# Kernel optimization log

Measured on AMD Instinct MI355X. Metric: run time of the kernel, lower is better.

The kernel has to match this reference:

```python
import jax, jax.numpy as jnp
import numpy as np

K = 5
TAU = 0.5
N = 8192
IN_DIM = 128
OUT_DIM = 128


def setup_inputs() -> dict:
    key = jax.random.key(0)
    k1, k2, k3 = jax.random.split(key, 3)
    x = jax.random.normal(k1, (N, IN_DIM), dtype=jnp.float32)
    laplacian = jax.random.normal(k2, (N, N), dtype=jnp.float32) / np.sqrt(N)
    # xavier-uniform-like init for theta (K, in_dim, out_dim)
    limit = np.sqrt(6.0 / (IN_DIM + OUT_DIM))
    theta = jax.random.uniform(k3, (K, IN_DIM, OUT_DIM), dtype=jnp.float32,
                               minval=-limit, maxval=limit)
    return {"x": x, "laplacian": laplacian, "theta": theta}


def _cheb_coeff(k_order: int, tau: float) -> jnp.ndarray:
    # c_k = (2/K) * exp(-tau * cos(pi*(k+0.5)/K)), Chebyshev-Gauss nodes
    ks = jnp.arange(k_order, dtype=jnp.float32)
    x_k = jnp.cos(jnp.pi * (ks + 0.5) / k_order)
    return (2.0 / k_order) * jnp.exp(-tau * x_k)


def reference(x, laplacian, theta):
    coeff = _cheb_coeff(K, TAU)  # (K,)
    # Chebyshev recurrence: T_0 = x, T_1 = L x, T_k = 2 L T_{k-1} - T_{k-2}
    tx_prev, tx_curr = x, laplacian @ x
    tx_list = [tx_prev, tx_curr]
    for _ in range(2, K):
        tx_next = 2.0 * (laplacian @ tx_curr) - tx_prev
        tx_list.append(tx_next)
        tx_prev, tx_curr = tx_curr, tx_next
    tx_stack = jnp.stack(tx_list, axis=0)  # (K, N, in_dim)
    return jnp.einsum('kni,kio,k->no', tx_stack, theta, coeff)
```

## Files before the change

### kernel.cpp

```cpp
#include <hip/hip_runtime.h>
#include <hip/hip_bf16.h>
#include <cmath>

#define NROWS 8192
#define DIM   128
#define KDIM  8192
#define BM    64
#define BN    128
#define BK    64
#define SPLITK 8
#define KCHUNK (KDIM / SPLITK)
#define GITERS (KCHUNK / BK)
#define LDSTRIDE 80

typedef __bf16 bf16_t;
typedef __bf16 bf16x8 __attribute__((ext_vector_type(8)));
typedef __bf16 bf16x4 __attribute__((ext_vector_type(4)));
typedef float  f32x4  __attribute__((ext_vector_type(4)));

__device__ __forceinline__ void async16(const void* g, void* l) {
    __builtin_amdgcn_global_load_lds(
        (const __attribute__((address_space(1))) unsigned int*)g,
        (__attribute__((address_space(3))) unsigned int*)l, 16, 0, 0);
}

__global__ void k_cvtL(const float* __restrict__ src, bf16_t* __restrict__ dst) {
    size_t i = ((size_t)blockIdx.x * 256 + threadIdx.x) * 8;
    float4 a = *(const float4*)(src + i);
    float4 b = *(const float4*)(src + i + 4);
    bf16x8 v;
    v[0] = (bf16_t)a.x; v[1] = (bf16_t)a.y; v[2] = (bf16_t)a.z; v[3] = (bf16_t)a.w;
    v[4] = (bf16_t)b.x; v[5] = (bf16_t)b.y; v[6] = (bf16_t)b.z; v[7] = (bf16_t)b.w;
    *(bf16x8*)(dst + i) = v;
}

__global__ void k_theta(const float* __restrict__ th, bf16_t* __restrict__ out,
                        float c0, float c1, float c2, float c3, float c4) {
    int idx = blockIdx.x * 256 + threadIdx.x;
    int k = idx >> 14;
    int o = (idx >> 7) & 127;
    int i = idx & 127;
    float c = (k == 0) ? c0 : (k == 1) ? c1 : (k == 2) ? c2 : (k == 3) ? c3 : c4;
    out[idx] = (bf16_t)(c * th[(k << 14) + (i << 7) + o]);
}

__global__ __launch_bounds__(256, 3)
void k_gemm(const bf16_t* __restrict__ A, const bf16_t* __restrict__ Bt,
            float* __restrict__ partial) {
    __shared__ __align__(16) bf16_t As[2][BM * BK];
    __shared__ __align__(16) bf16_t Bs[2][BN * BK];

    const int t     = threadIdx.x;
    const int mTile = blockIdx.x & 127;
    const int s     = blockIdx.x >> 7;
    const int mb    = mTile * BM;
    const int k0base = s * KCHUNK;
    const int wave = t >> 6, lane = t & 63;
    const int wM = (wave & 1) * 32;
    const int wN = (wave >> 1) * 64;
    const int lm = lane & 15, lk = lane >> 4;
    const int lrow = lane >> 3;
    const int lsrc = (lane & 7) ^ lrow;

    f32x4 acc[2][4];
#pragma unroll
    for (int a = 0; a < 2; ++a)
#pragma unroll
        for (int b = 0; b < 4; ++b) acc[a][b] = (f32x4)0.0f;

    auto stage = [&](int kk, int buf) {
        const int k0 = k0base + kk * BK;
#pragma unroll
        for (int i = 0; i < 2; ++i) {
            const int r = wave * 16 + i * 8 + lrow;
            async16(A + (size_t)(mb + r) * KDIM + k0 + lsrc * 8,
                    &As[buf][(wave * 16 + i * 8) * BK]);
        }
#pragma unroll
        for (int i = 0; i < 4; ++i) {
            const int n = wave * 32 + i * 8 + lrow;
            async16(Bt + (size_t)n * KDIM + k0 + lsrc * 8,
                    &Bs[buf][(wave * 32 + i * 8) * BK]);
        }
    };

    stage(0, 0);
    __syncthreads();
    for (int kk = 0; kk < GITERS; ++kk) {
        const int buf = kk & 1;
        if (kk + 1 < GITERS) stage(kk + 1, buf ^ 1);
#pragma unroll
        for (int ko = 0; ko < 2; ++ko) {
            bf16x8 af[2], bfr[4];
            const int csX = (ko * 4 + lk) ^ (lm & 7);
#pragma unroll
            for (int tm = 0; tm < 2; ++tm) {
                const int r = wM + tm * 16 + lm;
                af[tm] = *(const bf16x8*)(&As[buf][r * BK + csX * 8]);
            }
#pragma unroll
            for (int tn = 0; tn < 4; ++tn) {
                const int n = wN + tn * 16 + lm;
                bfr[tn] = *(const bf16x8*)(&Bs[buf][n * BK + csX * 8]);
            }
#pragma unroll
            for (int tm = 0; tm < 2; ++tm)
#pragma unroll
                for (int tn = 0; tn < 4; ++tn)
                    acc[tm][tn] = __builtin_amdgcn_mfma_f32_16x16x32_bf16(
                        af[tm], bfr[tn], acc[tm][tn], 0, 0, 0);
        }
        __syncthreads();
    }

    float* pOut = partial + (size_t)s * NROWS * DIM;
#pragma unroll
    for (int tm = 0; tm < 2; ++tm)
#pragma unroll
        for (int tn = 0; tn < 4; ++tn)
#pragma unroll
            for (int r = 0; r < 4; ++r) {
                const int row = mb + wM + tm * 16 + lk * 4 + r;
                const int col = wN + tn * 16 + lm;
                pOut[(size_t)row * DIM + col] = acc[tm][tn][r];
            }
}

template <int MODE>
__global__ void k_combine(const float* __restrict__ src, const float* __restrict__ prev,
                          float* __restrict__ f32dst, bf16_t* __restrict__ tbf,
                          bf16_t* __restrict__ bt) {
    __shared__ bf16_t tl[128 * 24];
    const size_t S = (size_t)NROWS * DIM;
    const int t  = threadIdx.x;
    const int n0 = blockIdx.x * 16;
    const int nl = t >> 4;
    const int dp = (t & 15) * 8;
    const int n  = n0 + nl;

    float y[8];
    if (MODE == 0) {
        float4 a = *(const float4*)(src + (size_t)n * DIM + dp);
        float4 b = *(const float4*)(src + (size_t)n * DIM + dp + 4);
        y[0] = a.x; y[1] = a.y; y[2] = a.z; y[3] = a.w;
        y[4] = b.x; y[5] = b.y; y[6] = b.z; y[7] = b.w;
    } else {
#pragma unroll
        for (int j = 0; j < 8; ++j) y[j] = 0.0f;
#pragma unroll
        for (int ss = 0; ss < SPLITK; ++ss) {
            const float* p = src + (size_t)ss * S + (size_t)n * DIM + dp;
            float4 a = *(const float4*)p;
            float4 b = *(const float4*)(p + 4);
            y[0] += a.x; y[1] += a.y; y[2] += a.z; y[3] += a.w;
            y[4] += b.x; y[5] += b.y; y[6] += b.z; y[7] += b.w;
        }
        if (MODE == 2) {
            float4 a = *(const float4*)(prev + (size_t)n * DIM + dp);
            float4 b = *(const float4*)(prev + (size_t)n * DIM + dp + 4);
            y[0] = 2.0f * y[0] - a.x; y[1] = 2.0f * y[1] - a.y;
            y[2] = 2.0f * y[2] - a.z; y[3] = 2.0f * y[3] - a.w;
            y[4] = 2.0f * y[4] - b.x; y[5] = 2.0f * y[5] - b.y;
            y[6] = 2.0f * y[6] - b.z; y[7] = 2.0f * y[7] - b.w;
        }
    }
    if (f32dst) {
        float4 a, b;
        a.x = y[0]; a.y = y[1]; a.z = y[2]; a.w = y[3];
        b.x = y[4]; b.y = y[5]; b.z = y[6]; b.w = y[7];
        *(float4*)(f32dst + (size_t)n * DIM + dp) = a;
        *(float4*)(f32dst + (size_t)n * DIM + dp + 4) = b;
    }
    bf16x8 v;
#pragma unroll
    for (int j = 0; j < 8; ++j) v[j] = (bf16_t)y[j];
    *(bf16x8*)(tbf + (size_t)n * DIM + dp) = v;
    if (bt) {
#pragma unroll
        for (int j = 0; j < 8; ++j) tl[(dp + j) * 24 + nl] = v[j];
        __syncthreads();
        const int d = t >> 1, h = (t & 1) * 8;
        bf16x8 w = *(const bf16x8*)(&tl[d * 24 + h]);
        *(bf16x8*)(bt + (size_t)d * NROWS + n0 + h) = w;
    }
}

__global__ __launch_bounds__(256, 2)
void k_proj(const bf16_t* __restrict__ T, const bf16_t* __restrict__ W,
            float* __restrict__ out) {
    __shared__ __align__(16) bf16_t As[BM * LDSTRIDE];
    __shared__ __align__(16) bf16_t Bs[BN * LDSTRIDE];

    const int t  = threadIdx.x;
    const int mb = blockIdx.x * BM;
    const int wave = t >> 6, lane = t & 63;
    const int wM = (wave & 1) * 32;
    const int wN = (wave >> 1) * 64;
    const int lm = lane & 15, lk = lane >> 4;
    const int arow = t >> 3;
    const int asc  = t & 7;
    const size_t S = (size_t)NROWS * DIM;

    f32x4 acc[2][4];
#pragma unroll
    for (int a = 0; a < 2; ++a)
#pragma unroll
        for (int b = 0; b < 4; ++b) acc[a][b] = (f32x4)0.0f;

    bf16x8 aR[2], bR[4];

    auto loadT = [&](int it) {
        const int seg = it >> 1;
        const int h   = (it & 1) * 64;
#pragma unroll
        for (int rep = 0; rep < 2; ++rep) {
            const int r = rep * 32 + arow;
            aR[rep] = *(const bf16x8*)(T + (size_t)seg * S +
                        (size_t)(mb + r) * DIM + h + asc * 8);
        }
#pragma unroll
        for (int rep = 0; rep < 4; ++rep) {
            const int o = rep * 32 + arow;
            bR[rep] = *(const bf16x8*)(W + seg * 16384 + o * 128 + h + asc * 8);
        }
    };
    auto storeT = [&]() {
#pragma unroll
        for (int rep = 0; rep < 2; ++rep) {
            const int r = rep * 32 + arow;
            *(bf16x8*)(&As[r * LDSTRIDE + asc * 8]) = aR[rep];
        }
#pragma unroll
        for (int rep = 0; rep < 4; ++rep) {
            const int o = rep * 32 + arow;
            *(bf16x8*)(&Bs[o * LDSTRIDE + asc * 8]) = bR[rep];
        }
    };

    loadT(0);
    for (int it = 0; it < 10; ++it) {
        __syncthreads();
        storeT();
        __syncthreads();
        if (it + 1 < 10) loadT(it + 1);
#pragma unroll
        for (int ko = 0; ko < 2; ++ko) {
            bf16x8 af[2], bfr[4];
#pragma unroll
            for (int tm = 0; tm < 2; ++tm)
                af[tm] = *(const bf16x8*)(&As[(wM + tm * 16 + lm) * LDSTRIDE +
                                              (ko * 4 + lk) * 8]);
#pragma unroll
            for (int tn = 0; tn < 4; ++tn)
                bfr[tn] = *(const bf16x8*)(&Bs[(wN + tn * 16 + lm) * LDSTRIDE +
                                               (ko * 4 + lk) * 8]);
#pragma unroll
            for (int tm = 0; tm < 2; ++tm)
#pragma unroll
                for (int tn = 0; tn < 4; ++tn)
                    acc[tm][tn] = __builtin_amdgcn_mfma_f32_16x16x32_bf16(
                        af[tm], bfr[tn], acc[tm][tn], 0, 0, 0);
        }
    }
#pragma unroll
    for (int tm = 0; tm < 2; ++tm)
#pragma unroll
        for (int tn = 0; tn < 4; ++tn)
#pragma unroll
            for (int r = 0; r < 4; ++r) {
                const int row = mb + wM + tm * 16 + lk * 4 + r;
                const int col = wN + tn * 16 + lm;
                out[(size_t)row * DIM + col] = acc[tm][tn][r];
            }
}

extern "C" void kernel_launch(void* const* d_in, const int* in_sizes, int n_in,
                              void* d_out, int out_size, void* d_ws, size_t ws_size,
                              hipStream_t stream) {
    const float* x  = nullptr;
    const float* L  = nullptr;
    const float* th = nullptr;
    for (int i = 0; i < n_in; ++i) {
        if (in_sizes[i] == NROWS * KDIM)       L  = (const float*)d_in[i];
        else if (in_sizes[i] == NROWS * DIM)   x  = (const float*)d_in[i];
        else if (in_sizes[i] == 5 * DIM * DIM) th = (const float*)d_in[i];
    }
    float* out = (float*)d_out;

    const size_t S = (size_t)NROWS * DIM;
    char* ws = (char*)d_ws;
    size_t off = 0;
    auto alloc = [&](size_t bytes) {
        void* p = ws + off;
        off = (off + bytes + 255) & ~(size_t)255;
        return p;
    };
    bf16_t* Tbf     = (bf16_t*)alloc(5 * S * 2);
    bf16_t* Bt      = (bf16_t*)alloc(5 * S * 2);
    float*  Tf32    = (float*)alloc(2 * S * 4);
    bf16_t* thT     = (bf16_t*)alloc(5 * 128 * 128 * 2);
    float*  partial = (float*)alloc((size_t)SPLITK * S * 4);
    bf16_t* Lbf     = (bf16_t*)alloc((size_t)NROWS * KDIM * 2);
    if (off > ws_size) return;

    float c[5];
    for (int k = 0; k < 5; ++k)
        c[k] = (float)((2.0 / 5.0) * exp(-0.5 * cos(M_PI * (k + 0.5) / 5.0)));

    dim3 blk(256);
    k_cvtL<<<32768, blk, 0, stream>>>(L, Lbf);
    k_combine<0><<<512, blk, 0, stream>>>(x, nullptr, nullptr, Tbf, Bt);
    k_theta<<<320, blk, 0, stream>>>(th, thT, c[0], c[1], c[2], c[3], c[4]);

    for (int j = 1; j <= 4; ++j) {
        k_gemm<<<1024, blk, 0, stream>>>(Lbf, Bt + (size_t)(j - 1) * S, partial);
        bf16_t* tbf = Tbf + (size_t)j * S;
        bf16_t* bt  = (j < 4) ? Bt + (size_t)j * S : nullptr;
        if (j == 1)
            k_combine<1><<<512, blk, 0, stream>>>(partial, nullptr, Tf32 + S, tbf, bt);
        else if (j == 2)
            k_combine<2><<<512, blk, 0, stream>>>(partial, x, Tf32, tbf, bt);
        else if (j == 3)
            k_combine<2><<<512, blk, 0, stream>>>(partial, Tf32 + S, Tf32 + S, tbf, bt);
        else
            k_combine<2><<<512, blk, 0, stream>>>(partial, Tf32, nullptr, tbf, nullptr);
    }
    k_proj<<<128, blk, 0, stream>>>(Tbf, thT, out);
}
```

Baseline: 604.1 us.

## Fuse fp32-to-bf16 Laplacian conversion into first GEMM and retile split-K

```diff
diff --git a/kernel.cpp b/kernel.cpp
--- a/kernel.cpp
+++ b/kernel.cpp
@@ -5,33 +5,23 @@
 #define NROWS 8192
 #define DIM   128
 #define KDIM  8192
-#define BM    64
+#define BM    32
 #define BN    128
 #define BK    64
-#define SPLITK 8
+#define SPLITK 4
 #define KCHUNK (KDIM / SPLITK)
 #define GITERS (KCHUNK / BK)
+#define MTILES (NROWS / BM)
 #define LDSTRIDE 80
 
 typedef __bf16 bf16_t;
 typedef __bf16 bf16x8 __attribute__((ext_vector_type(8)));
-typedef __bf16 bf16x4 __attribute__((ext_vector_type(4)));
 typedef float  f32x4  __attribute__((ext_vector_type(4)));
 
 __device__ __forceinline__ void async16(const void* g, void* l) {
     __builtin_amdgcn_global_load_lds(
         (const __attribute__((address_space(1))) unsigned int*)g,
         (__attribute__((address_space(3))) unsigned int*)l, 16, 0, 0);
-}
-
-__global__ void k_cvtL(const float* __restrict__ src, bf16_t* __restrict__ dst) {
-    size_t i = ((size_t)blockIdx.x * 256 + threadIdx.x) * 8;
-    float4 a = *(const float4*)(src + i);
-    float4 b = *(const float4*)(src + i + 4);
-    bf16x8 v;
-    v[0] = (bf16_t)a.x; v[1] = (bf16_t)a.y; v[2] = (bf16_t)a.z; v[3] = (bf16_t)a.w;
-    v[4] = (bf16_t)b.x; v[5] = (bf16_t)b.y; v[6] = (bf16_t)b.z; v[7] = (bf16_t)b.w;
-    *(bf16x8*)(dst + i) = v;
 }
 
 __global__ void k_theta(const float* __restrict__ th, bf16_t* __restrict__ out,
@@ -44,38 +34,34 @@
     out[idx] = (bf16_t)(c * th[(k << 14) + (i << 7) + o]);
 }
 
-__global__ __launch_bounds__(256, 3)
-void k_gemm(const bf16_t* __restrict__ A, const bf16_t* __restrict__ Bt,
-            float* __restrict__ partial) {
+template <int MODE>
+__global__ __launch_bounds__(256, 4)
+void k_gemm(const void* __restrict__ Ap, const bf16_t* __restrict__ Bt,
+            float* __restrict__ partial, bf16_t* __restrict__ Lbf_out) {
     __shared__ __align__(16) bf16_t As[2][BM * BK];
     __shared__ __align__(16) bf16_t Bs[2][BN * BK];
 
     const int t     = threadIdx.x;
-    const int mTile = blockIdx.x & 127;
-    const int s     = blockIdx.x >> 7;
+    const int mTile = blockIdx.x & (MTILES - 1);
+    const int s     = blockIdx.x >> 8;
     const int mb    = mTile * BM;
     const int k0base = s * KCHUNK;
     const int wave = t >> 6, lane = t & 63;
-    const int wM = (wave & 1) * 32;
+    const int wM = (wave & 1) * 16;
     const int wN = (wave >> 1) * 64;
     const int lm = lane & 15, lk = lane >> 4;
     const int lrow = lane >> 3;
     const int lsrc = (lane & 7) ^ lrow;
-
-    f32x4 acc[2][4];
-#pragma unroll
-    for (int a = 0; a < 2; ++a)
-#pragma unroll
-        for (int b = 0; b < 4; ++b) acc[a][b] = (f32x4)0.0f;
-
-    auto stage = [&](int kk, int buf) {
+    const int rA   = wave * 8 + lrow;
+
+    f32x4 acc[4];
+#pragma unroll
+    for (int b = 0; b < 4; ++b) acc[b] = (f32x4)0.0f;
+
+    float4 RA[2][2];
+
+    auto stageB = [&](int kk, int buf) {
         const int k0 = k0base + kk * BK;
-#pragma unroll
-        for (int i = 0; i < 2; ++i) {
-            const int r = wave * 16 + i * 8 + lrow;
-            async16(A + (size_t)(mb + r) * KDIM + k0 + lsrc * 8,
-                    &As[buf][(wave * 16 + i * 8) * BK]);
-        }
 #pragma unroll
         for (int i = 0; i < 4; ++i) {
             const int n = wave * 32 + i * 8 + lrow;
@@ -83,47 +69,72 @@
                     &Bs[buf][(wave * 32 + i * 8) * BK]);
         }
     };
-
-    stage(0, 0);
-    __syncthreads();
-    for (int kk = 0; kk < GITERS; ++kk) {
-        const int buf = kk & 1;
-        if (kk + 1 < GITERS) stage(kk + 1, buf ^ 1);
+    auto stageA0 = [&](int kk, int buf) {
+        const int k0 = k0base + kk * BK;
+        async16((const bf16_t*)Ap + (size_t)(mb + rA) * KDIM + k0 + lsrc * 8,
+                &As[buf][wave * 8 * BK]);
+    };
+    auto loadA2 = [&](int kk, int p) {
+        const int k0 = k0base + kk * BK;
+        const float* base = (const float*)Ap + (size_t)(mb + rA) * KDIM + k0 + lsrc * 8;
+        RA[p][0] = *(const float4*)base;
+        RA[p][1] = *(const float4*)(base + 4);
+    };
+    auto writeA2 = [&](int kk, int buf, int p) {
+        bf16x8 v;
+        v[0] = (bf16_t)RA[p][0].x; v[1] = (bf16_t)RA[p][0].y;
+        v[2] = (bf16_t)RA[p][0].z; v[3] = (bf16_t)RA[p][0].w;
+        v[4] = (bf16_t)RA[p][1].x; v[5] = (bf16_t)RA[p][1].y;
+        v[6] = (bf16_t)RA[p][1].z; v[7] = (bf16_t)RA[p][1].w;
+        *(bf16x8*)(&As[buf][rA * BK + (lane & 7) * 8]) = v;
+        const int k0 = k0base + kk * BK;
+        *(bf16x8*)(Lbf_out + (size_t)(mb + rA) * KDIM + k0 + lsrc * 8) = v;
+    };
+
+    auto compute = [&](int buf) {
 #pragma unroll
         for (int ko = 0; ko < 2; ++ko) {
-            bf16x8 af[2], bfr[4];
             const int csX = (ko * 4 + lk) ^ (lm & 7);
-#pragma unroll
-            for (int tm = 0; tm < 2; ++tm) {
-                const int r = wM + tm * 16 + lm;
-                af[tm] = *(const bf16x8*)(&As[buf][r * BK + csX * 8]);
-            }
-#pragma unroll
-            for (int tn = 0; tn < 4; ++tn) {
-                const int n = wN + tn * 16 + lm;
-                bfr[tn] = *(const bf16x8*)(&Bs[buf][n * BK + csX * 8]);
-            }
-#pragma unroll
-            for (int tm = 0; tm < 2; ++tm)
-#pragma unroll
-                for (int tn = 0; tn < 4; ++tn)
-                    acc[tm][tn] = __builtin_amdgcn_mfma_f32_16x16x32_bf16(
-                        af[tm], bfr[tn], acc[tm][tn], 0, 0, 0);
-        }
-        __syncthreads();
+            bf16x8 af = *(const bf16x8*)(&As[buf][(wM + lm) * BK + csX * 8]);
+            bf16x8 bfr[4];
+#pragma unroll
+            for (int tn = 0; tn < 4; ++tn)
+                bfr[tn] = *(const bf16x8*)(&Bs[buf][(wN + tn * 16 + lm) * BK + csX * 8]);
+#pragma unroll
+            for (int tn = 0; tn < 4; ++tn)
+                acc[tn] = __builtin_amdgcn_mfma_f32_16x16x32_bf16(
+                    af, bfr[tn], acc[tn], 0, 0, 0);
+        }
+    };
+
+    if (MODE == 0) {
+        stageA0(0, 0); stageB(0, 0);
+        for (int kk = 0; kk < GITERS; ++kk) {
+            const int buf = kk & 1;
+            __syncthreads();
+            if (kk + 1 < GITERS) { stageA0(kk + 1, buf ^ 1); stageB(kk + 1, buf ^ 1); }
+            compute(buf);
+        }
+    } else {
+        loadA2(0, 0); stageB(0, 0);
+        for (int kk = 0; kk < GITERS; ++kk) {
+            const int buf = kk & 1;
+            writeA2(kk, buf, kk & 1);
+            __syncthreads();
+            if (kk + 1 < GITERS) { loadA2(kk + 1, (kk + 1) & 1); stageB(kk + 1, buf ^ 1); }
+            compute(buf);
+        }
     }
 
     float* pOut = partial + (size_t)s * NROWS * DIM;
 #pragma unroll
-    for (int tm = 0; tm < 2; ++tm)
-#pragma unroll
-        for (int tn = 0; tn < 4; ++tn)
-#pragma unroll
-            for (int r = 0; r < 4; ++r) {
-                const int row = mb + wM + tm * 16 + lk * 4 + r;
-                const int col = wN + tn * 16 + lm;
-                pOut[(size_t)row * DIM + col] = acc[tm][tn][r];
-            }
+    for (int tn = 0; tn < 4; ++tn)
+#pragma unroll
+        for (int r = 0; r < 4; ++r) {
+            const int row = mb + wM + lk * 4 + r;
+            const int col = wN + tn * 16 + lm;
+            pOut[(size_t)row * DIM + col] = acc[tn][r];
+        }
 }
 
 template <int MODE>
@@ -188,11 +199,11 @@
 __global__ __launch_bounds__(256, 2)
 void k_proj(const bf16_t* __restrict__ T, const bf16_t* __restrict__ W,
             float* __restrict__ out) {
-    __shared__ __align__(16) bf16_t As[BM * LDSTRIDE];
-    __shared__ __align__(16) bf16_t Bs[BN * LDSTRIDE];
+    __shared__ __align__(16) bf16_t As[64 * LDSTRIDE];
+    __shared__ __align__(16) bf16_t Bs[128 * LDSTRIDE];
 
     const int t  = threadIdx.x;
-    const int mb = blockIdx.x * BM;
+    const int mb = blockIdx.x * 64;
     const int wave = t >> 6, lane = t & 63;
     const int wM = (wave & 1) * 32;
     const int wN = (wave >> 1) * 64;
@@ -308,12 +319,15 @@
         c[k] = (float)((2.0 / 5.0) * exp(-0.5 * cos(M_PI * (k + 0.5) / 5.0)));
 
     dim3 blk(256);
-    k_cvtL<<<32768, blk, 0, stream>>>(L, Lbf);
+    k_theta<<<320, blk, 0, stream>>>(th, thT, c[0], c[1], c[2], c[3], c[4]);
     k_combine<0><<<512, blk, 0, stream>>>(x, nullptr, nullptr, Tbf, Bt);
-    k_theta<<<320, blk, 0, stream>>>(th, thT, c[0], c[1], c[2], c[3], c[4]);
 
     for (int j = 1; j <= 4; ++j) {
-        k_gemm<<<1024, blk, 0, stream>>>(Lbf, Bt + (size_t)(j - 1) * S, partial);
+        const bf16_t* Bj = Bt + (size_t)(j - 1) * S;
+        if (j == 1)
+            k_gemm<2><<<MTILES * SPLITK, blk, 0, stream>>>(L, Bj, partial, Lbf);
+        else
+            k_gemm<0><<<MTILES * SPLITK, blk, 0, stream>>>(Lbf, Bj, partial, nullptr);
         bf16_t* tbf = Tbf + (size_t)j * S;
         bf16_t* bt  = (j < 4) ? Bt + (size_t)j * S : nullptr;
         if (j == 1)
```

New measurement: 631.8 us. 1.05x slower.

## Replace LDS-staged GEMM with direct-to-register loads and larger per-wave tiles

Applied to the files above, without the earlier changes.

```diff
diff --git a/kernel.cpp b/kernel.cpp
--- a/kernel.cpp
+++ b/kernel.cpp
@@ -5,24 +5,17 @@
 #define NROWS 8192
 #define DIM   128
 #define KDIM  8192
-#define BM    64
-#define BN    128
-#define BK    64
 #define SPLITK 8
 #define KCHUNK (KDIM / SPLITK)
+#define BK    64
 #define GITERS (KCHUNK / BK)
+#define BMB   128
+#define MTILES (NROWS / BMB)
 #define LDSTRIDE 80
 
 typedef __bf16 bf16_t;
 typedef __bf16 bf16x8 __attribute__((ext_vector_type(8)));
-typedef __bf16 bf16x4 __attribute__((ext_vector_type(4)));
 typedef float  f32x4  __attribute__((ext_vector_type(4)));
-
-__device__ __forceinline__ void async16(const void* g, void* l) {
-    __builtin_amdgcn_global_load_lds(
-        (const __attribute__((address_space(1))) unsigned int*)g,
-        (__attribute__((address_space(3))) unsigned int*)l, 16, 0, 0);
-}
 
 __global__ void k_cvtL(const float* __restrict__ src, bf16_t* __restrict__ dst) {
     size_t i = ((size_t)blockIdx.x * 256 + threadIdx.x) * 8;
@@ -44,85 +37,73 @@
     out[idx] = (bf16_t)(c * th[(k << 14) + (i << 7) + o]);
 }
 
-__global__ __launch_bounds__(256, 3)
-void k_gemm(const bf16_t* __restrict__ A, const bf16_t* __restrict__ Bt,
-            float* __restrict__ partial) {
-    __shared__ __align__(16) bf16_t As[2][BM * BK];
-    __shared__ __align__(16) bf16_t Bs[2][BN * BK];
-
+__global__ void k_gemm(const bf16_t* __restrict__ A, const bf16_t* __restrict__ Bt,
+                       float* __restrict__ partial) {
     const int t     = threadIdx.x;
-    const int mTile = blockIdx.x & 127;
-    const int s     = blockIdx.x >> 7;
-    const int mb    = mTile * BM;
+    const int mTile = blockIdx.x & (MTILES - 1);
+    const int s     = blockIdx.x >> 6;
+    const int wave  = t >> 6, lane = t & 63;
+    const int lm = lane & 15, lk = lane >> 4;
+    const int row0   = mTile * BMB + wave * 32;
     const int k0base = s * KCHUNK;
-    const int wave = t >> 6, lane = t & 63;
-    const int wM = (wave & 1) * 32;
-    const int wN = (wave >> 1) * 64;
-    const int lm = lane & 15, lk = lane >> 4;
-    const int lrow = lane >> 3;
-    const int lsrc = (lane & 7) ^ lrow;
-
-    f32x4 acc[2][4];
-#pragma unroll
-    for (int a = 0; a < 2; ++a)
-#pragma unroll
-        for (int b = 0; b < 4; ++b) acc[a][b] = (f32x4)0.0f;
-
-    auto stage = [&](int kk, int buf) {
+
+    f32x4 acc[2][8];
+#pragma unroll
+    for (int rg = 0; rg < 2; ++rg)
+#pragma unroll
+        for (int cg = 0; cg < 8; ++cg) acc[rg][cg] = (f32x4)0.0f;
+
+    const bf16_t* a0 = A + (size_t)(row0 + lm) * KDIM + lk * 8;
+    const bf16_t* a1 = A + (size_t)(row0 + 16 + lm) * KDIM + lk * 8;
+    const bf16_t* bb = Bt + (size_t)lm * KDIM + lk * 8;
+
+    auto loadA = [&](int kk, bf16x8 aF[2][2]) {
         const int k0 = k0base + kk * BK;
 #pragma unroll
-        for (int i = 0; i < 2; ++i) {
-            const int r = wave * 16 + i * 8 + lrow;
-            async16(A + (size_t)(mb + r) * KDIM + k0 + lsrc * 8,
-                    &As[buf][(wave * 16 + i * 8) * BK]);
-        }
-#pragma unroll
-        for (int i = 0; i < 4; ++i) {
-            const int n = wave * 32 + i * 8 + lrow;
-            async16(Bt + (size_t)n * KDIM + k0 + lsrc * 8,
-                    &Bs[buf][(wave * 32 + i * 8) * BK]);
+        for (int ko = 0; ko < 2; ++ko) {
+            aF[0][ko] = *(const bf16x8*)(a0 + k0 + ko * 32);
+            aF[1][ko] = *(const bf16x8*)(a1 + k0 + ko * 32);
         }
     };
 
-    stage(0, 0);
-    __syncthreads();
+    bf16x8 aF[2][2];
+    loadA(0, aF);
+
+#pragma unroll 2
     for (int kk = 0; kk < GITERS; ++kk) {
-        const int buf = kk & 1;
-        if (kk + 1 < GITERS) stage(kk + 1, buf ^ 1);
+        const int k0 = k0base + kk * BK;
+        bf16x8 aN[2][2];
+        if (kk + 1 < GITERS) loadA(kk + 1, aN);
 #pragma unroll
         for (int ko = 0; ko < 2; ++ko) {
-            bf16x8 af[2], bfr[4];
-            const int csX = (ko * 4 + lk) ^ (lm & 7);
-#pragma unroll
-            for (int tm = 0; tm < 2; ++tm) {
-                const int r = wM + tm * 16 + lm;
-                af[tm] = *(const bf16x8*)(&As[buf][r * BK + csX * 8]);
+            bf16x8 bq[8];
+#pragma unroll
+            for (int cg = 0; cg < 8; ++cg)
+                bq[cg] = *(const bf16x8*)(bb + (size_t)cg * 16 * KDIM + k0 + ko * 32);
+#pragma unroll
+            for (int cg = 0; cg < 8; ++cg) {
+                acc[0][cg] = __builtin_amdgcn_mfma_f32_16x16x32_bf16(
+                    aF[0][ko], bq[cg], acc[0][cg], 0, 0, 0);
+                acc[1][cg] = __builtin_amdgcn_mfma_f32_16x16x32_bf16(
+                    aF[1][ko], bq[cg], acc[1][cg], 0, 0, 0);
             }
-#pragma unroll
-            for (int tn = 0; tn < 4; ++tn) {
-                const int n = wN + tn * 16 + lm;
-                bfr[tn] = *(const bf16x8*)(&Bs[buf][n * BK + csX * 8]);
-            }
-#pragma unroll
-            for (int tm = 0; tm < 2; ++tm)
-#pragma unroll
-                for (int tn = 0; tn < 4; ++tn)
-                    acc[tm][tn] = __builtin_amdgcn_mfma_f32_16x16x32_bf16(
-                        af[tm], bfr[tn], acc[tm][tn], 0, 0, 0);
-        }
-        __syncthreads();
+        }
+#pragma unroll
+        for (int rg = 0; rg < 2; ++rg)
+#pragma unroll
+            for (int ko = 0; ko < 2; ++ko) aF[rg][ko] = aN[rg][ko];
     }
 
     float* pOut = partial + (size_t)s * NROWS * DIM;
 #pragma unroll
-    for (int tm = 0; tm < 2; ++tm)
-#pragma unroll
-        for (int tn = 0; tn < 4; ++tn)
+    for (int rg = 0; rg < 2; ++rg)
+#pragma unroll
+        for (int cg = 0; cg < 8; ++cg)
 #pragma unroll
             for (int r = 0; r < 4; ++r) {
-                const int row = mb + wM + tm * 16 + lk * 4 + r;
-                const int col = wN + tn * 16 + lm;
-                pOut[(size_t)row * DIM + col] = acc[tm][tn][r];
+                const int row = row0 + rg * 16 + lk * 4 + r;
+                const int col = cg * 16 + lm;
+                pOut[(size_t)row * DIM + col] = acc[rg][cg][r];
             }
 }
 
@@ -188,11 +169,11 @@
 __global__ __launch_bounds__(256, 2)
 void k_proj(const bf16_t* __restrict__ T, const bf16_t* __restrict__ W,
             float* __restrict__ out) {
-    __shared__ __align__(16) bf16_t As[BM * LDSTRIDE];
-    __shared__ __align__(16) bf16_t Bs[BN * LDSTRIDE];
+    __shared__ __align__(16) bf16_t As[64 * LDSTRIDE];
+    __shared__ __align__(16) bf16_t Bs[128 * LDSTRIDE];
 
     const int t  = threadIdx.x;
-    const int mb = blockIdx.x * BM;
+    const int mb = blockIdx.x * 64;
     const int wave = t >> 6, lane = t & 63;
     const int wM = (wave & 1) * 32;
     const int wN = (wave >> 1) * 64;
@@ -292,7 +273,7 @@
     size_t off = 0;
     auto alloc = [&](size_t bytes) {
         void* p = ws + off;
-        off = (off + bytes + 255) & ~(size_t)255;
+        off = (off + bytes + 1023) & ~(size_t)1023;
         return p;
     };
     bf16_t* Tbf     = (bf16_t*)alloc(5 * S * 2);
@@ -309,11 +290,12 @@
 
     dim3 blk(256);
     k_cvtL<<<32768, blk, 0, stream>>>(L, Lbf);
+    k_theta<<<320, blk, 0, stream>>>(th, thT, c[0], c[1], c[2], c[3], c[4]);
     k_combine<0><<<512, blk, 0, stream>>>(x, nullptr, nullptr, Tbf, Bt);
-    k_theta<<<320, blk, 0, stream>>>(th, thT, c[0], c[1], c[2], c[3], c[4]);
 
     for (int j = 1; j <= 4; ++j) {
-        k_gemm<<<1024, blk, 0, stream>>>(Lbf, Bt + (size_t)(j - 1) * S, partial);
+        const bf16_t* Bj = Bt + (size_t)(j - 1) * S;
+        k_gemm<<<MTILES * SPLITK, blk, 0, stream>>>(Lbf, Bj, partial);
         bf16_t* tbf = Tbf + (size_t)j * S;
         bf16_t* bt  = (j < 4) ? Bt + (size_t)j * S : nullptr;
         if (j == 1)
```

Measured after the change: 762.9 us. 26.3% more time.
